# Kernel optimization log

Measured on AMD Instinct MI355X. Metric: run time of the kernel, lower is better.

The kernel has to match this reference:

```python
import jax, jax.numpy as jnp
import numpy as np

D_MODEL = 768; N_LAYERS = 12; D_STATE = 128; D_CONV = 4; HEADDIM = 64
D_INNER = 2 * D_MODEL            # 1536
NHEADS = D_INNER // HEADDIM      # 24
CONV_DIM = D_INNER + 2 * D_STATE # 1792
D_IN_PROJ = 2 * D_INNER + 2 * D_STATE + NHEADS  # 3352
D_FF = 2048; VOCAB = 32000; BATCH = 2; SEQ = 2048
EPS = 1e-5


def setup_inputs() -> dict:
    key = jax.random.key(0)
    ks = jax.random.split(key, 20)
    s = 0.02
    inp = {
        'input_ids': jax.random.randint(ks[0], (BATCH, SEQ), 0, VOCAB),
        'emb':    jax.random.normal(ks[1], (VOCAB, D_MODEL)) * s,
        'ln_w':   jnp.ones((N_LAYERS, D_MODEL)),
        'ln_b':   jnp.zeros((N_LAYERS, D_MODEL)),
        'in_w':   jax.random.normal(ks[2], (N_LAYERS, D_IN_PROJ, D_MODEL)) * s,
        'conv_w': jax.random.normal(ks[3], (N_LAYERS, CONV_DIM, D_CONV)) * 0.1,
        'conv_b': jnp.zeros((N_LAYERS, CONV_DIM)),
        'dt_bias': jax.random.normal(ks[4], (N_LAYERS, NHEADS)) * 0.5,
        'A_log':  jnp.log(1.0 + jax.random.uniform(ks[5], (N_LAYERS, NHEADS)) * 15.0),
        'Dp':     jnp.ones((N_LAYERS, NHEADS)),
        'rms_w':  jnp.ones((N_LAYERS, D_INNER)),
        'out_w':  jax.random.normal(ks[6], (N_LAYERS, D_MODEL, D_INNER)) * s,
        'mlp_ln_w': jnp.ones((N_LAYERS, D_MODEL)),
        'mlp_ln_b': jnp.zeros((N_LAYERS, D_MODEL)),
        'w1':     jax.random.normal(ks[7], (N_LAYERS, D_FF, D_MODEL)) * s,
        'w2':     jax.random.normal(ks[8], (N_LAYERS, D_FF, D_MODEL)) * s,
        'w3':     jax.random.normal(ks[9], (N_LAYERS, D_MODEL, D_FF)) * s,
        'normf_w': jnp.ones((D_MODEL,)),
        'normf_b': jnp.zeros((D_MODEL,)),
        'lm_w':   jax.random.normal(ks[10], (VOCAB, D_MODEL)) * s,
    }
    return inp


def layer_norm(x, w, b):
    mu = jnp.mean(x, -1, keepdims=True)
    xc = x - mu
    var = jnp.mean(xc * xc, -1, keepdims=True)
    return xc * jax.lax.rsqrt(var + EPS) * w + b


def mamba_mixer(h, in_w, conv_w, conv_b, dt_bias, A_log, Dp, rms_w, out_w):
    b, l, _ = h.shape
    zxbcdt = jnp.einsum('bld,ed->ble', h, in_w)                 # [b,l,3352]
    z = zxbcdt[..., :D_INNER]
    xBC = zxbcdt[..., D_INNER:D_INNER + CONV_DIM]
    dt = jax.nn.softplus(zxbcdt[..., D_INNER + CONV_DIM:] + dt_bias)  # [b,l,nh]
    # causal depthwise conv1d over time, kernel D_CONV, then silu
    xpad = jnp.pad(xBC, ((0, 0), (D_CONV - 1, 0), (0, 0)))
    conv = conv_b
    for k in range(D_CONV):
        conv = conv + conv_w[:, k] * xpad[:, k:k + l, :]
    xBC = jax.nn.silu(conv)
    x = xBC[..., :D_INNER].reshape(b, l, NHEADS, HEADDIM)
    Bm = xBC[..., D_INNER:D_INNER + D_STATE]                    # [b,l,n] (ngroups=1)
    Cm = xBC[..., D_INNER + D_STATE:]                           # [b,l,n]
    A = -jnp.exp(A_log)                                         # [nh]
    dA = jnp.exp(dt * A)                                        # [b,l,nh]
    dtB = dt[..., None] * Bm[:, :, None, :]                     # [b,l,nh,n]

    def step(state, inputs):
        dA_t, dtB_t, x_t, C_t = inputs
        state = state * dA_t[..., None, None] + dtB_t[:, :, None, :] * x_t[..., None]
        y_t = jnp.einsum('bhpn,bn->bhp', state, C_t)
        return state, y_t

    state0 = jnp.zeros((b, NHEADS, HEADDIM, D_STATE), dtype=h.dtype)
    xs = (jnp.moveaxis(dA, 1, 0), jnp.moveaxis(dtB, 1, 0),
          jnp.moveaxis(x, 1, 0), jnp.moveaxis(Cm, 1, 0))
    _, ys = jax.lax.scan(step, state0, xs)
    y = jnp.moveaxis(ys, 0, 1) + Dp[None, None, :, None] * x    # [b,l,nh,hd]
    y = y.reshape(b, l, D_INNER)
    # gated RMSNorm (norm_before_gate=False)
    y = y * jax.nn.silu(z)
    y = y * jax.lax.rsqrt(jnp.mean(y * y, -1, keepdims=True) + EPS) * rms_w
    return jnp.einsum('ble,de->bld', y, out_w)


def reference(input_ids, emb, ln_w, ln_b, in_w, conv_w, conv_b, dt_bias, A_log, Dp,
              rms_w, out_w, mlp_ln_w, mlp_ln_b, w1, w2, w3, normf_w, normf_b, lm_w):
    h = emb[input_ids]                                          # [b,l,d]
    for i in range(N_LAYERS):
        resid = h
        hn = layer_norm(resid, ln_w[i], ln_b[i])
        hm = mamba_mixer(hn, in_w[i], conv_w[i], conv_b[i], dt_bias[i],
                         A_log[i], Dp[i], rms_w[i], out_w[i])
        hf = hm + resid
        g = layer_norm(hf, mlp_ln_w[i], mlp_ln_b[i])
        h = hf + jnp.einsum('blf,df->bld', jax.nn.silu(jnp.einsum('bld,fd->blf', g, w1[i])) *
                            jnp.einsum('bld,fd->blf', g, w2[i]), w3[i])
    h = layer_norm(h, normf_w, normf_b)
    return jnp.einsum('bld,vd->blv', h, lm_w)
```

## Files before the change

### kernel.cpp

```cpp
#include <hip/hip_runtime.h>
#include <cstdint>
#include <cstddef>

#define TOK    4096
#define SEQL   2048
#define DMODEL 768
#define NLAYER 12
#define DSTATE 128
#define HEADD  64
#define DINNER 1536
#define NHEADS 24
#define CONVD  1792
#define DIPROJ 3352
#define DIPAD  3456
#define DFF    2048
#define VOCABN 32000
#define NCHUNK 16
#define CHUNKL 128
#define CTS    8

typedef __attribute__((ext_vector_type(8))) short bf16x8;
typedef __attribute__((ext_vector_type(4))) float f32x4;

__device__ __forceinline__ unsigned short f2bf(float f) {
  union { float f; unsigned u; } v; v.f = f;
  return (unsigned short)((v.u + 0x7FFFu + ((v.u >> 16) & 1u)) >> 16);
}

__device__ __forceinline__ void gld16(const void* g, void* l) {
  __builtin_amdgcn_global_load_lds(
      (const __attribute__((address_space(1))) unsigned int*)g,
      (__attribute__((address_space(3))) unsigned int*)l, 16, 0, 0);
}

__device__ __forceinline__ void stream_store(float* addr, float v) {
  asm volatile("global_store_dword %0, %1, off sc0 sc1 nt" :: "v"(addr), "v"(v) : "memory");
}

template <int NW>
__device__ __forceinline__ void red2t(float& a, float& b) {
#pragma unroll
  for (int o = 1; o < 64; o <<= 1) { a += __shfl_xor(a, o, 64); b += __shfl_xor(b, o, 64); }
  __shared__ float sa[NW], sb[NW];
  const int w = threadIdx.x >> 6;
  if ((threadIdx.x & 63) == 0) { sa[w] = a; sb[w] = b; }
  __syncthreads();
  a = sa[0]; b = sb[0];
#pragma unroll
  for (int i = 1; i < NW; ++i) { a += sa[i]; b += sb[i]; }
}

template <int NW>
__device__ __forceinline__ float red1t(float a) {
#pragma unroll
  for (int o = 1; o < 64; o <<= 1) a += __shfl_xor(a, o, 64);
  __shared__ float sa[NW];
  const int w = threadIdx.x >> 6;
  if ((threadIdx.x & 63) == 0) sa[w] = a;
  __syncthreads();
  float r = sa[0];
#pragma unroll
  for (int i = 1; i < NW; ++i) r += sa[i];
  return r;
}

template <int EPI, int BM, int BN>
__global__ __launch_bounds__(256, 2) void gemm_bt(
    const unsigned short* __restrict__ A, const unsigned short* __restrict__ B,
    float* __restrict__ C, unsigned short* __restrict__ Cg,
    const float* __restrict__ R, int M, int N, int K) {
  constexpr int WM  = BM / 2, WN = BN / 2;
  constexpr int MFR = WM / 16, NFR = WN / 16;
  constexpr int LPS = (BM == 256 ? 4 : BM == 128 ? 2 : 1) + (BN == 128 ? 2 : 1);
  __shared__ unsigned short lA[2][BM * 32];
  __shared__ unsigned short lB[2][BN * 32];

  int lid = (int)blockIdx.x;
  {
    const int nwg = (int)gridDim.x;
    const int xcd = lid & 7;
    const int q = nwg >> 3, r = nwg & 7;
    const int b2 = (xcd < r) ? xcd * (q + 1) : r * (q + 1) + (xcd - r) * q;
    lid = b2 + (lid >> 3);
  }
  const int mtiles = M / BM;
  int m0, n0;
  if constexpr (BM >= 128 && BN == 128) {
    constexpr int GRP = (BM == 256) ? 8 : 16;
    const int nt = (int)gridDim.x / mtiles;
    const int span = GRP * nt;
    const int g = lid / span, rem = lid % span;
    m0 = (g * GRP + (rem % GRP)) * BM;
    n0 = (rem / GRP) * BN;
  } else {
    m0 = (lid % mtiles) * BM;
    n0 = (lid / mtiles) * BN;
  }

  const int tid = threadIdx.x, wave = tid >> 6, lane = tid & 63;
  const int wr = (wave >> 1) * WM, wc = (wave & 1) * WN;
  const int srow = lane >> 2;
  const int scol = (((lane & 3) ^ ((lane >> 3) & 3))) * 8;
  const int rdk  = ((lane >> 4) ^ ((lane >> 1) & 3)) * 8;

  f32x4 acc[MFR][NFR];
#pragma unroll
  for (int i = 0; i < MFR; ++i)
#pragma unroll
    for (int j = 0; j < NFR; ++j) acc[i][j] = (f32x4){0.f, 0.f, 0.f, 0.f};

  const size_t arow0 = (size_t)(m0 + (BM == 256 ? wave * 64 : BM == 128 ? wave * 32 : wave * 16) + srow) * K + scol;
  const size_t brow0 = (size_t)(n0 + (BN == 128 ? wave * 32 : wave * 16) + srow) * K + scol;

  auto stage = [&](int buf, int k0) {
    if constexpr (BM == 256) {
#pragma unroll
      for (int j = 0; j < 4; ++j)
        gld16(A + arow0 + (size_t)(j * 16) * K + k0, lA[buf] + (wave * 4 + j) * 512);
    } else if constexpr (BM == 128) {
      gld16(A + arow0 + k0,                  lA[buf] + (wave * 2 + 0) * 512);
      gld16(A + arow0 + (size_t)16 * K + k0, lA[buf] + (wave * 2 + 1) * 512);
    } else {
      gld16(A + arow0 + k0, lA[buf] + wave * 512);
    }
    if constexpr (BN == 128) {
      gld16(B + brow0 + k0,                  lB[buf] + (wave * 2 + 0) * 512);
      gld16(B + brow0 + (size_t)16 * K + k0, lB[buf] + (wave * 2 + 1) * 512);
    } else {
      gld16(B + brow0 + k0, lB[buf] + wave * 512);
    }
  };

  stage(0, 0);
  stage(1, 32);
  int cur = 0;
  for (int k0 = 0; k0 < K; k0 += 32) {
    asm volatile("s_waitcnt vmcnt(%0)" :: "i"(LPS) : "memory");
    __builtin_amdgcn_s_barrier();
    bf16x8 af[MFR], bfr[NFR];
#pragma unroll
    for (int mi = 0; mi < MFR; ++mi) {
      const int ra = wr + mi * 16 + (lane & 15);
      af[mi] = *(const bf16x8*)&lA[cur][ra * 32 + rdk];
    }
#pragma unroll
    for (int ni = 0; ni < NFR; ++ni) {
      const int rb = wc + ni * 16 + (lane & 15);
      bfr[ni] = *(const bf16x8*)&lB[cur][rb * 32 + rdk];
    }
    asm volatile("s_waitcnt lgkmcnt(0)" ::: "memory");
    __builtin_amdgcn_sched_barrier(0);
    __builtin_amdgcn_s_barrier();
    if (k0 + 64 < K) stage(cur, k0 + 64);
    __builtin_amdgcn_sched_barrier(0);
#pragma unroll
    for (int mi = 0; mi < MFR; ++mi)
#pragma unroll
      for (int ni = 0; ni < NFR; ++ni)
        acc[mi][ni] = __builtin_amdgcn_mfma_f32_16x16x32_bf16(af[mi], bfr[ni], acc[mi][ni], 0, 0, 0);
    cur ^= 1;
  }

  const int er = (lane >> 4) * 4, ec = lane & 15;
#pragma unroll
  for (int mi = 0; mi < MFR; ++mi) {
#pragma unroll
    for (int r = 0; r < 4; ++r) {
      const size_t row = (size_t)(m0 + wr + mi * 16 + er + r);
#pragma unroll
      for (int ni = 0; ni < NFR; ++ni) {
        float v = acc[mi][ni][r];
        const int col = n0 + wc + ec + ni * 16;
        if constexpr (EPI == 2) {
          const float o = __shfl_xor(v, 1, 64);
          if ((lane & 1) == 0)
            Cg[row * DFF + (col >> 1)] = f2bf((v / (1.f + expf(-v))) * o);
        } else if constexpr (EPI == 1) {
          C[row * N + col] = v + R[row * N + col];
        } else if constexpr (EPI == 3) {
          stream_store(&C[row * N + col], v);
        } else {
          C[row * N + col] = v;
        }
      }
    }
  }
}

__global__ __launch_bounds__(256) void cvt_k(const float* __restrict__ in, unsigned short* __restrict__ out, long n) {
  const long i = ((long)blockIdx.x * 256 + threadIdx.x) * 4;
  if (i >= n) return;
  const float4 v = *(const float4*)(in + i);
  ushort4 o; o.x = f2bf(v.x); o.y = f2bf(v.y); o.z = f2bf(v.z); o.w = f2bf(v.w);
  *(ushort4*)(out + i) = o;
}

__global__ __launch_bounds__(256) void cvt_inw_k(const float* __restrict__ in, unsigned short* __restrict__ out) {
  const int row = blockIdx.x;
  const int l = row / DIPAD, n = row % DIPAD;
  unsigned short* orow = out + (size_t)row * DMODEL;
  if (n >= DIPROJ) {
    for (int c = threadIdx.x; c < DMODEL; c += 256) orow[c] = 0;
    return;
  }
  const float* irow = in + ((size_t)l * DIPROJ + n) * DMODEL;
  for (int c = threadIdx.x; c < DMODEL; c += 256) orow[c] = f2bf(irow[c]);
}

__global__ __launch_bounds__(256) void cvt_w12_k(const float* __restrict__ w1, const float* __restrict__ w2,
                                                 unsigned short* __restrict__ out) {
  const int row = blockIdx.x;
  const int l = row / (2 * DFF), rr = row % (2 * DFF);
  const int f = rr >> 1;
  const float* irow = ((rr & 1) == 0) ? (w1 + ((size_t)l * DFF + f) * DMODEL)
                                      : (w2 + ((size_t)l * DFF + f) * DMODEL);
  unsigned short* orow = out + (size_t)row * DMODEL;
  for (int c = threadIdx.x; c < DMODEL; c += 256) orow[c] = f2bf(irow[c]);
}

__global__ __launch_bounds__(192) void embed_k(const int* __restrict__ ids, const float* __restrict__ emb, float* __restrict__ h) {
  const int t = blockIdx.x;
  const float4 v = *(const float4*)(emb + (size_t)ids[t] * DMODEL + threadIdx.x * 4);
  *(float4*)(h + (size_t)t * DMODEL + threadIdx.x * 4) = v;
}

__global__ __launch_bounds__(192) void ln_k(const float* __restrict__ x, const float* __restrict__ w, const float* __restrict__ b,
                                            unsigned short* __restrict__ out) {
  const int t = blockIdx.x, c4 = threadIdx.x * 4;
  const float4 v = *(const float4*)(x + (size_t)t * DMODEL + c4);
  float s = v.x + v.y + v.z + v.w;
  float ss = v.x * v.x + v.y * v.y + v.z * v.z + v.w * v.w;
  red2t<3>(s, ss);
  const float mu = s * (1.f / DMODEL);
  const float inv = rsqrtf(ss * (1.f / DMODEL) - mu * mu + 1e-5f);
  const float4 wv = *(const float4*)(w + c4);
  const float4 bv = *(const float4*)(b + c4);
  ushort4 o;
  o.x = f2bf((v.x - mu) * inv * wv.x + bv.x);
  o.y = f2bf((v.y - mu) * inv * wv.y + bv.y);
  o.z = f2bf((v.z - mu) * inv * wv.z + bv.z);
  o.w = f2bf((v.w - mu) * inv * wv.w + bv.w);
  *(ushort4*)(out + (size_t)t * DMODEL + c4) = o;
}

__global__ __launch_bounds__(448) void conv_k(const float* __restrict__ zx, const float* __restrict__ cw, const float* __restrict__ cb,
                                              const float* __restrict__ dt_bias, const float* __restrict__ A_log,
                                              float* __restrict__ xs, float* __restrict__ Bm, float* __restrict__ Cm,
                                              float* __restrict__ dtv, float* __restrict__ dAv) {
  const int t0g = blockIdx.x * CTS;
  const int b = t0g >> 11, l0 = t0g & (SEQL - 1);
  const int c4 = threadIdx.x * 4;
  const float4 w0  = *(const float4*)(cw + c4 * 4);
  const float4 w1v = *(const float4*)(cw + c4 * 4 + 4);
  const float4 w2v = *(const float4*)(cw + c4 * 4 + 8);
  const float4 w3v = *(const float4*)(cw + c4 * 4 + 12);
  const float4 bias = *(const float4*)(cb + c4);
  float4 win[3];
#pragma unroll
  for (int j = 0; j < 3; ++j) {
    const int ll = l0 - 3 + j;
    win[j] = (ll >= 0) ? *(const float4*)(zx + (size_t)(b * SEQL + ll) * DIPAD + DINNER + c4)
                       : (float4){0.f, 0.f, 0.f, 0.f};
  }
#pragma unroll
  for (int i = 0; i < CTS; ++i) {
    const int t = t0g + i;
    const float4 cur4 = *(const float4*)(zx + (size_t)t * DIPAD + DINNER + c4);
    float4 a = bias;
    a.x = fmaf(w0.x,  win[0].x, a.x); a.y = fmaf(w1v.x, win[0].y, a.y);
    a.z = fmaf(w2v.x, win[0].z, a.z); a.w = fmaf(w3v.x, win[0].w, a.w);
    a.x = fmaf(w0.y,  win[1].x, a.x); a.y = fmaf(w1v.y, win[1].y, a.y);
    a.z = fmaf(w2v.y, win[1].z, a.z); a.w = fmaf(w3v.y, win[1].w, a.w);
    a.x = fmaf(w0.z,  win[2].x, a.x); a.y = fmaf(w1v.z, win[2].y, a.y);
    a.z = fmaf(w2v.z, win[2].z, a.z); a.w = fmaf(w3v.z, win[2].w, a.w);
    a.x = fmaf(w0.w,  cur4.x, a.x);   a.y = fmaf(w1v.w, cur4.y, a.y);
    a.z = fmaf(w2v.w, cur4.z, a.z);   a.w = fmaf(w3v.w, cur4.w, a.w);
    a.x = a.x / (1.f + expf(-a.x));
    a.y = a.y / (1.f + expf(-a.y));
    a.z = a.z / (1.f + expf(-a.z));
    a.w = a.w / (1.f + expf(-a.w));
    if (threadIdx.x < 384)      *(float4*)(xs + (size_t)t * DINNER + c4) = a;
    else if (threadIdx.x < 416) *(float4*)(Bm + (size_t)t * DSTATE + (c4 - DINNER)) = a;
    else                        *(float4*)(Cm + (size_t)t * DSTATE + (c4 - DINNER - DSTATE)) = a;
    win[0] = win[1]; win[1] = win[2]; win[2] = cur4;
  }
  if (threadIdx.x < NHEADS) {
    const int hh = threadIdx.x;
    const float eA = expf(A_log[hh]);
    const float db = dt_bias[hh];
#pragma unroll
    for (int i = 0; i < CTS; ++i) {
      const int t = t0g + i;
      const float xv = zx[(size_t)t * DIPAD + DINNER + CONVD + hh] + db;
      const float dt = (xv > 20.f) ? xv : log1pf(expf(xv));
      dtv[t * NHEADS + hh] = dt;
      dAv[t * NHEADS + hh] = expf(-dt * eA);
    }
  }
}

__global__ __launch_bounds__(256) void scan1_k(const float* __restrict__ xs, const float* __restrict__ Bm, const float* __restrict__ Cm,
                                               const float* __restrict__ dtv, const float* __restrict__ dAv,
                                               const float* __restrict__ Dp, float* __restrict__ y,
                                               float* __restrict__ Sloc, float* __restrict__ cumv) {
  __shared__ float lB[2][16][128];
  __shared__ float lC[2][16][128];
  __shared__ float sdA[2][16], sdt[2][16];
  const int pg = blockIdx.x, hh = blockIdx.y, z = blockIdx.z;
  const int b = z >> 4, c = z & (NCHUNK - 1);
  const int pl = threadIdx.x >> 4, ln = threadIdx.x & 15;
  const int p = pg * 16 + pl;
  const int wv = threadIdx.x >> 6, lane = threadIdx.x & 63;
  const float Dph = Dp[hh];
  const int bT = b * SEQL + c * CHUNKL;

  auto stage = [&](int buf, int t0) {
#pragma unroll
    for (int j = 0; j < 2; ++j) {
      const int pr = wv + 4 * j;
      const int row = 2 * pr + (lane >> 5);
      gld16(Bm + (size_t)(t0 + row) * DSTATE + (lane & 31) * 4, &lB[buf][2 * pr][0]);
      gld16(Cm + (size_t)(t0 + row) * DSTATE + (lane & 31) * 4, &lC[buf][2 * pr][0]);
    }
    if (threadIdx.x < 16)      sdA[buf][threadIdx.x]      = dAv[(t0 + threadIdx.x) * NHEADS + hh];
    else if (threadIdx.x < 32) sdt[buf][threadIdx.x - 16] = dtv[(t0 + threadIdx.x - 16) * NHEADS + hh];
  };

  float s0 = 0, s1 = 0, s2 = 0, s3 = 0, s4 = 0, s5 = 0, s6 = 0, s7 = 0;
  float r = 1.f;
  int cur = 0;
  stage(0, bT);
  for (int cc = 0; cc < CHUNKL; cc += 16) {
    const int t0 = bT + cc;
    __builtin_amdgcn_s_barrier();
    float xq[16];
#pragma unroll
    for (int i = 0; i < 16; ++i) xq[i] = xs[(size_t)(t0 + i) * DINNER + hh * HEADD + p];
    if (cc + 16 < CHUNKL) stage(cur ^ 1, t0 + 16);
    asm volatile("s_waitcnt vmcnt(4) lgkmcnt(0)" ::: "memory");
    __builtin_amdgcn_s_barrier();
#pragma unroll
    for (int i = 0; i < 16; ++i) {
      const float dAt = sdA[cur][i], dtt = sdt[cur][i];
      const float xdt = xq[i] * dtt;
      const float4 B0 = *(const float4*)&lB[cur][i][ln * 4];
      const float4 B1 = *(const float4*)&lB[cur][i][64 + ln * 4];
      const float4 C0 = *(const float4*)&lC[cur][i][ln * 4];
      const float4 C1 = *(const float4*)&lC[cur][i][64 + ln * 4];
      float yp;
      s0 = fmaf(s0, dAt, B0.x * xdt); yp = s0 * C0.x;
      s1 = fmaf(s1, dAt, B0.y * xdt); yp = fmaf(s1, C0.y, yp);
      s2 = fmaf(s2, dAt, B0.z * xdt); yp = fmaf(s2, C0.z, yp);
      s3 = fmaf(s3, dAt, B0.w * xdt); yp = fmaf(s3, C0.w, yp);
      s4 = fmaf(s4, dAt, B1.x * xdt); yp = fmaf(s4, C1.x, yp);
      s5 = fmaf(s5, dAt, B1.y * xdt); yp = fmaf(s5, C1.y, yp);
      s6 = fmaf(s6, dAt, B1.z * xdt); yp = fmaf(s6, C1.z, yp);
      s7 = fmaf(s7, dAt, B1.w * xdt); yp = fmaf(s7, C1.w, yp);
#pragma unroll
      for (int o = 1; o < 16; o <<= 1) yp += __shfl_xor(yp, o, 64);
      if (ln == 0) y[(size_t)(t0 + i) * DINNER + hh * HEADD + p] = fmaf(Dph, xq[i], yp);
      r *= dAt;
      if (threadIdx.x == 0) cumv[(size_t)(b * NHEADS + hh) * SEQL + (c * CHUNKL + cc + i)] = r;
    }
    cur ^= 1;
  }
  float* sp = Sloc + (((size_t)(b * NHEADS + hh) * NCHUNK + c) * HEADD + p) * DSTATE;
  *(float4*)(sp + ln * 4)      = (float4){s0, s1, s2, s3};
  *(float4*)(sp + 64 + ln * 4) = (float4){s4, s5, s6, s7};
}

__global__ __launch_bounds__(256) void scan3_k(const float* __restrict__ Cm, const float* __restrict__ cumv,
                                               const float* __restrict__ Sloc, float* __restrict__ y) {
  __shared__ float lC[2][16][128];
  __shared__ float sCum[2][16];
  const int pg = blockIdx.x, hh = blockIdx.y, z = blockIdx.z;
  const int b = z / (NCHUNK - 1), c = z % (NCHUNK - 1) + 1;
  const int pl = threadIdx.x >> 4, ln = threadIdx.x & 15;
  const int p = pg * 16 + pl;
  const int wv = threadIdx.x >> 6, lane = threadIdx.x & 63;
  const int bT = b * SEQL + c * CHUNKL;

  float4 sA = (float4){0.f, 0.f, 0.f, 0.f}, sB = (float4){0.f, 0.f, 0.f, 0.f};
  {
    const float* spb = Sloc + ((size_t)(b * NHEADS + hh) * NCHUNK) * (HEADD * DSTATE) + (size_t)p * DSTATE;
    for (int j = 1; j <= c; ++j) {
      const float Pj = cumv[(size_t)(b * NHEADS + hh) * SEQL + j * CHUNKL - 1];
      const float* sj = spb + (size_t)(j - 1) * (HEADD * DSTATE);
      const float4 v0 = *(const float4*)(sj + ln * 4);
      const float4 v1 = *(const float4*)(sj + 64 + ln * 4);
      sA.x = fmaf(Pj, sA.x, v0.x); sA.y = fmaf(Pj, sA.y, v0.y);
      sA.z = fmaf(Pj, sA.z, v0.z); sA.w = fmaf(Pj, sA.w, v0.w);
      sB.x = fmaf(Pj, sB.x, v1.x); sB.y = fmaf(Pj, sB.y, v1.y);
      sB.z = fmaf(Pj, sB.z, v1.z); sB.w = fmaf(Pj, sB.w, v1.w);
    }
  }

  auto stage = [&](int buf, int t0) {
#pragma unroll
    for (int j = 0; j < 2; ++j) {
      const int pr = wv + 4 * j;
      const int row = 2 * pr + (lane >> 5);
      gld16(Cm + (size_t)(t0 + row) * DSTATE + (lane & 31) * 4, &lC[buf][2 * pr][0]);
    }
    if (threadIdx.x < 16)
      sCum[buf][threadIdx.x] = cumv[(size_t)(b * NHEADS + hh) * SEQL + (t0 - b * SEQL) + threadIdx.x];
  };

  int cur = 0;
  stage(0, bT);
  for (int cc = 0; cc < CHUNKL; cc += 16) {
    const int t0 = bT + cc;
    __builtin_amdgcn_s_barrier();
    float yq[16];
#pragma unroll
    for (int i = 0; i < 16; ++i) yq[i] = y[(size_t)(t0 + i) * DINNER + hh * HEADD + p];
    if (cc + 16 < CHUNKL) stage(cur ^ 1, t0 + 16);
    asm volatile("s_waitcnt vmcnt(2) lgkmcnt(0)" ::: "memory");
    __builtin_amdgcn_s_barrier();
#pragma unroll
    for (int i = 0; i < 16; ++i) {
      const float4 C0 = *(const float4*)&lC[cur][i][ln * 4];
      const float4 C1 = *(const float4*)&lC[cur][i][64 + ln * 4];
      float yp = sA.x * C0.x;
      yp = fmaf(sA.y, C0.y, yp);
      yp = fmaf(sA.z, C0.z, yp);
      yp = fmaf(sA.w, C0.w, yp);
      yp = fmaf(sB.x, C1.x, yp);
      yp = fmaf(sB.y, C1.y, yp);
      yp = fmaf(sB.z, C1.z, yp);
      yp = fmaf(sB.w, C1.w, yp);
#pragma unroll
      for (int o = 1; o < 16; o <<= 1) yp += __shfl_xor(yp, o, 64);
      if (ln == 0) y[(size_t)(t0 + i) * DINNER + hh * HEADD + p] = fmaf(sCum[cur][i], yp, yq[i]);
    }
    cur ^= 1;
  }
}

__global__ __launch_bounds__(384) void grms_k(const float* __restrict__ y, const float* __restrict__ zx,
                                              const float* __restrict__ rw, unsigned short* __restrict__ out) {
  const int t = blockIdx.x, c4 = threadIdx.x * 4;
  const float4 yv = *(const float4*)(y + (size_t)t * DINNER + c4);
  const float4 zv = *(const float4*)(zx + (size_t)t * DIPAD + c4);
  float4 g;
  g.x = yv.x * (zv.x / (1.f + expf(-zv.x)));
  g.y = yv.y * (zv.y / (1.f + expf(-zv.y)));
  g.z = yv.z * (zv.z / (1.f + expf(-zv.z)));
  g.w = yv.w * (zv.w / (1.f + expf(-zv.w)));
  float ss = g.x * g.x + g.y * g.y + g.z * g.z + g.w * g.w;
  ss = red1t<6>(ss);
  const float inv = rsqrtf(ss * (1.f / DINNER) + 1e-5f);
  const float4 rv = *(const float4*)(rw + c4);
  ushort4 o;
  o.x = f2bf(g.x * inv * rv.x);
  o.y = f2bf(g.y * inv * rv.y);
  o.z = f2bf(g.z * inv * rv.z);
  o.w = f2bf(g.w * inv * rv.w);
  *(ushort4*)(out + (size_t)t * DINNER + c4) = o;
}

extern "C" void kernel_launch(void* const* d_in, const int* in_sizes, int n_in,
                              void* d_out, int out_size, void* d_ws, size_t ws_size,
                              hipStream_t stream) {
  const int*   ids      = (const int*)  d_in[0];
  const float* emb      = (const float*)d_in[1];
  const float* ln_w     = (const float*)d_in[2];
  const float* ln_b     = (const float*)d_in[3];
  const float* in_w     = (const float*)d_in[4];
  const float* conv_w   = (const float*)d_in[5];
  const float* conv_b   = (const float*)d_in[6];
  const float* dt_bias  = (const float*)d_in[7];
  const float* A_log    = (const float*)d_in[8];
  const float* Dp       = (const float*)d_in[9];
  const float* rms_w    = (const float*)d_in[10];
  const float* out_w    = (const float*)d_in[11];
  const float* mlp_ln_w = (const float*)d_in[12];
  const float* mlp_ln_b = (const float*)d_in[13];
  const float* w1       = (const float*)d_in[14];
  const float* w2       = (const float*)d_in[15];
  const float* w3       = (const float*)d_in[16];
  const float* normf_w  = (const float*)d_in[17];
  const float* normf_b  = (const float*)d_in[18];
  const float* lm_w     = (const float*)d_in[19];

  char* base = (char*)d_ws;
  size_t off = 0;
  auto alloc = [&](size_t bytes) -> char* {
    char* p = base + off;
    off += (bytes + 255) & ~(size_t)255;
    return p;
  };
  float* h             = (float*)alloc((size_t)TOK * DMODEL * 4);
  unsigned short* xn   = (unsigned short*)alloc((size_t)TOK * DMODEL * 2);
  float* zx            = (float*)alloc((size_t)TOK * DIPAD * 4);
  float* xs            = (float*)alloc((size_t)TOK * DINNER * 4);
  float* Bm            = (float*)alloc((size_t)TOK * DSTATE * 4);
  float* Cm            = (float*)alloc((size_t)TOK * DSTATE * 4);
  float* dtv           = (float*)alloc((size_t)TOK * NHEADS * 4);
  float* dAv           = (float*)alloc((size_t)TOK * NHEADS * 4);
  float* y             = (float*)alloc((size_t)TOK * DINNER * 4);
  unsigned short* ybf  = (unsigned short*)alloc((size_t)TOK * DINNER * 2);
  float* hf            = (float*)alloc((size_t)TOK * DMODEL * 4);
  unsigned short* gbf  = (unsigned short*)alloc((size_t)TOK * DMODEL * 2);
  unsigned short* gate = (unsigned short*)alloc((size_t)TOK * DFF * 2);
  float* Sloc          = (float*)alloc((size_t)2 * NHEADS * NCHUNK * HEADD * DSTATE * 4);
  float* cumv          = (float*)alloc((size_t)2 * NHEADS * SEQL * 4);
  unsigned short* inw_bf  = (unsigned short*)alloc((size_t)NLAYER * DIPAD * DMODEL * 2);
  unsigned short* outw_bf = (unsigned short*)alloc((size_t)NLAYER * DMODEL * DINNER * 2);
  unsigned short* w12_bf  = (unsigned short*)alloc((size_t)NLAYER * 2 * DFF * DMODEL * 2);
  unsigned short* w3_bf   = (unsigned short*)alloc((size_t)NLAYER * DMODEL * DFF * 2);
  unsigned short* lm_bf   = (unsigned short*)alloc((size_t)VOCABN * DMODEL * 2);
  if (off > ws_size) return;

  cvt_inw_k<<<NLAYER * DIPAD, 256, 0, stream>>>(in_w, inw_bf);
  cvt_w12_k<<<NLAYER * 2 * DFF, 256, 0, stream>>>(w1, w2, w12_bf);
  {
    const long n1 = (long)NLAYER * DMODEL * DINNER;
    cvt_k<<<(unsigned)((n1 + 1023) / 1024), 256, 0, stream>>>(out_w, outw_bf, n1);
    const long n3 = (long)NLAYER * DMODEL * DFF;
    cvt_k<<<(unsigned)((n3 + 1023) / 1024), 256, 0, stream>>>(w3, w3_bf, n3);
    const long n4 = (long)VOCABN * DMODEL;
    cvt_k<<<(unsigned)((n4 + 1023) / 1024), 256, 0, stream>>>(lm_w, lm_bf, n4);
  }

  embed_k<<<TOK, 192, 0, stream>>>(ids, emb, h);

  for (int l = 0; l < NLAYER; ++l) {
    ln_k<<<TOK, 192, 0, stream>>>(h, ln_w + l * DMODEL, ln_b + l * DMODEL, xn);
    gemm_bt<0, 256, 128><<<(TOK / 256) * (DIPAD / 128), 256, 0, stream>>>(
        xn, inw_bf + (size_t)l * DIPAD * DMODEL, zx, nullptr, nullptr, TOK, DIPAD, DMODEL);
    conv_k<<<TOK / CTS, 448, 0, stream>>>(zx, conv_w + (size_t)l * CONVD * 4, conv_b + (size_t)l * CONVD,
                                          dt_bias + l * NHEADS, A_log + l * NHEADS, xs, Bm, Cm, dtv, dAv);
    scan1_k<<<dim3(4, NHEADS, 2 * NCHUNK), 256, 0, stream>>>(xs, Bm, Cm, dtv, dAv, Dp + l * NHEADS, y, Sloc, cumv);
    scan3_k<<<dim3(4, NHEADS, 2 * (NCHUNK - 1)), 256, 0, stream>>>(Cm, cumv, Sloc, y);
    grms_k<<<TOK, 384, 0, stream>>>(y, zx, rms_w + (size_t)l * DINNER, ybf);
    gemm_bt<1, 128, 64><<<(TOK / 128) * (DMODEL / 64), 256, 0, stream>>>(
        ybf, outw_bf + (size_t)l * DMODEL * DINNER, hf, nullptr, h, TOK, DMODEL, DINNER);
    ln_k<<<TOK, 192, 0, stream>>>(hf, mlp_ln_w + l * DMODEL, mlp_ln_b + l * DMODEL, gbf);
    gemm_bt<2, 256, 128><<<(TOK / 256) * (2 * DFF / 128), 256, 0, stream>>>(
        gbf, w12_bf + (size_t)l * 2 * DFF * DMODEL, nullptr, gate, nullptr, TOK, 2 * DFF, DMODEL);
    gemm_bt<1, 128, 64><<<(TOK / 128) * (DMODEL / 64), 256, 0, stream>>>(
        gate, w3_bf + (size_t)l * DMODEL * DFF, h, nullptr, hf, TOK, DMODEL, DFF);
  }

  ln_k<<<TOK, 192, 0, stream>>>(h, normf_w, normf_b, xn);
  gemm_bt<3, 256, 128><<<(TOK / 256) * (VOCABN / 128), 256, 0, stream>>>(
      xn, lm_bf, (float*)d_out, nullptr, nullptr, TOK, VOCABN, DMODEL);
}
```

Before: 5.824 ms.

## Split-K the narrow out_proj and down-proj GEMMs with a separate reduction kernel

Adds an EPI==4 mode to the GEMM that splits K into two halves across twice as many blocks, writing partial results to a workspace buffer. A new reduction kernel sums the two partials with the residual. This targets the small-N (768) GEMMs whose grids underfill the GPU. It adds extra global memory traffic for partials and one more kernel launch per GEMM.

Measured after the change: 5.777 ms. No clear change (-0.8%).

```diff
diff --git a/kernel.cpp b/kernel.cpp
--- a/kernel.cpp
+++ b/kernel.cpp
@@ -83,6 +83,14 @@
     const int b2 = (xcd < r) ? xcd * (q + 1) : r * (q + 1) + (xcd - r) * q;
     lid = b2 + (lid >> 3);
   }
+  int sidx = 0, kbeg = 0, kend = K;
+  if constexpr (EPI == 4) {
+    const int nblk = (int)gridDim.x >> 1;
+    sidx = lid / nblk;
+    lid  = lid % nblk;
+    kbeg = sidx * (K >> 1);
+    kend = kbeg + (K >> 1);
+  }
   const int mtiles = M / BM;
   int m0, n0;
   if constexpr (BM >= 128 && BN == 128) {
@@ -131,10 +139,10 @@
     }
   };
 
-  stage(0, 0);
-  stage(1, 32);
+  stage(0, kbeg);
+  stage(1, kbeg + 32);
   int cur = 0;
-  for (int k0 = 0; k0 < K; k0 += 32) {
+  for (int k0 = kbeg; k0 < kend; k0 += 32) {
     asm volatile("s_waitcnt vmcnt(%0)" :: "i"(LPS) : "memory");
     __builtin_amdgcn_s_barrier();
     bf16x8 af[MFR], bfr[NFR];
@@ -151,7 +159,7 @@
     asm volatile("s_waitcnt lgkmcnt(0)" ::: "memory");
     __builtin_amdgcn_sched_barrier(0);
     __builtin_amdgcn_s_barrier();
-    if (k0 + 64 < K) stage(cur, k0 + 64);
+    if (k0 + 64 < kend) stage(cur, k0 + 64);
     __builtin_amdgcn_sched_barrier(0);
 #pragma unroll
     for (int mi = 0; mi < MFR; ++mi)
@@ -179,12 +187,28 @@
           C[row * N + col] = v + R[row * N + col];
         } else if constexpr (EPI == 3) {
           stream_store(&C[row * N + col], v);
+        } else if constexpr (EPI == 4) {
+          C[(size_t)sidx * M * N + row * N + col] = v;
         } else {
           C[row * N + col] = v;
         }
       }
     }
   }
+}
+
+__global__ __launch_bounds__(256) void red_k(const float* __restrict__ P, const float* __restrict__ R,
+                                             float* __restrict__ out) {
+  const size_t i = ((size_t)blockIdx.x * 256 + threadIdx.x) * 4;
+  const float4 a = *(const float4*)(P + i);
+  const float4 b = *(const float4*)(P + (size_t)TOK * DMODEL + i);
+  const float4 r = *(const float4*)(R + i);
+  float4 o;
+  o.x = a.x + b.x + r.x;
+  o.y = a.y + b.y + r.y;
+  o.z = a.z + b.z + r.z;
+  o.w = a.w + b.w + r.w;
+  *(float4*)(out + i) = o;
 }
 
 __global__ __launch_bounds__(256) void cvt_k(const float* __restrict__ in, unsigned short* __restrict__ out, long n) {
@@ -505,6 +529,7 @@
   unsigned short* gate = (unsigned short*)alloc((size_t)TOK * DFF * 2);
   float* Sloc          = (float*)alloc((size_t)2 * NHEADS * NCHUNK * HEADD * DSTATE * 4);
   float* cumv          = (float*)alloc((size_t)2 * NHEADS * SEQL * 4);
+  float* Cpart         = (float*)alloc((size_t)2 * TOK * DMODEL * 4);
   unsigned short* inw_bf  = (unsigned short*)alloc((size_t)NLAYER * DIPAD * DMODEL * 2);
   unsigned short* outw_bf = (unsigned short*)alloc((size_t)NLAYER * DMODEL * DINNER * 2);
   unsigned short* w12_bf  = (unsigned short*)alloc((size_t)NLAYER * 2 * DFF * DMODEL * 2);
@@ -534,13 +559,15 @@
     scan1_k<<<dim3(4, NHEADS, 2 * NCHUNK), 256, 0, stream>>>(xs, Bm, Cm, dtv, dAv, Dp + l * NHEADS, y, Sloc, cumv);
     scan3_k<<<dim3(4, NHEADS, 2 * (NCHUNK - 1)), 256, 0, stream>>>(Cm, cumv, Sloc, y);
     grms_k<<<TOK, 384, 0, stream>>>(y, zx, rms_w + (size_t)l * DINNER, ybf);
-    gemm_bt<1, 128, 64><<<(TOK / 128) * (DMODEL / 64), 256, 0, stream>>>(
-        ybf, outw_bf + (size_t)l * DMODEL * DINNER, hf, nullptr, h, TOK, DMODEL, DINNER);
+    gemm_bt<4, 128, 64><<<2 * (TOK / 128) * (DMODEL / 64), 256, 0, stream>>>(
+        ybf, outw_bf + (size_t)l * DMODEL * DINNER, Cpart, nullptr, nullptr, TOK, DMODEL, DINNER);
+    red_k<<<TOK * DMODEL / 1024, 256, 0, stream>>>(Cpart, h, hf);
     ln_k<<<TOK, 192, 0, stream>>>(hf, mlp_ln_w + l * DMODEL, mlp_ln_b + l * DMODEL, gbf);
     gemm_bt<2, 256, 128><<<(TOK / 256) * (2 * DFF / 128), 256, 0, stream>>>(
         gbf, w12_bf + (size_t)l * 2 * DFF * DMODEL, nullptr, gate, nullptr, TOK, 2 * DFF, DMODEL);
-    gemm_bt<1, 128, 64><<<(TOK / 128) * (DMODEL / 64), 256, 0, stream>>>(
-        gate, w3_bf + (size_t)l * DMODEL * DFF, h, nullptr, hf, TOK, DMODEL, DFF);
+    gemm_bt<4, 128, 64><<<2 * (TOK / 128) * (DMODEL / 64), 256, 0, stream>>>(
+        gate, w3_bf + (size_t)l * DMODEL * DFF, Cpart, nullptr, nullptr, TOK, DMODEL, DFF);
+    red_k<<<TOK * DMODEL / 1024, 256, 0, stream>>>(Cpart, hf, h);
   }
 
   ln_k<<<TOK, 192, 0, stream>>>(h, normf_w, normf_b, xn);
```
